# Performance work log

Hardware: AMD Instinct MI355X
Metric: run time of the kernel (lower is better)

Reference implementation:

```python
import jax, jax.numpy as jnp
import numpy as np

DIM = 192
HEADS = 6
HD = DIM // HEADS
MEM = 8
EMA = 0.99
MLP_H = int(DIM * 2.0)
SCALE = HD ** -0.5
EPS = 1e-5


def layer_norm(x, w, b):
    mu = x.mean(-1, keepdims=True)
    xc = x - mu
    var = (xc * xc).mean(-1, keepdims=True)
    return xc * jax.lax.rsqrt(var + EPS) * w + b


def setup_inputs() -> dict:
    key = jax.random.key(0)
    ks = jax.random.split(key, 16)
    B, H, W = 2, 96, 96
    x = jax.random.normal(ks[0], (B, H * W, DIM), jnp.float32)

    def lin(k, din, dout):
        kw, kb = jax.random.split(k)
        return (0.02 * jax.random.normal(kw, (din, dout), jnp.float32),
                0.02 * jax.random.normal(kb, (dout,), jnp.float32))

    wq, bq = lin(ks[1], DIM, DIM)
    wk, bk = lin(ks[2], DIM, DIM)
    wv, bv = lin(ks[3], DIM, DIM)
    wo, bo = lin(ks[4], DIM, DIM)
    w1, b1 = lin(ks[5], DIM, MLP_H)
    w2, b2 = lin(ks[6], MLP_H, DIM)
    ones = jnp.ones((DIM,), jnp.float32)
    zeros = jnp.zeros((DIM,), jnp.float32)
    return dict(x_bnc=x,
                ln_q_w=ones, ln_q_b=zeros,
                ln_kv_w=ones, ln_kv_b=zeros,
                wq=wq, bq=bq, wk=wk, bk=bk, wv=wv, bv=bv,
                wo=wo, bo=bo,
                ln2_w=ones, ln2_b=zeros,
                w1=w1, b1=b1, w2=w2, b2=b2,
                H=96, W=96)


def reference(x_bnc, ln_q_w, ln_q_b, ln_kv_w, ln_kv_b,
              wq, bq, wk, bk, wv, bv, wo, bo,
              ln2_w, ln2_b, w1, b1, w2, b2, H, W):
    B, N, C = x_bnc.shape

    # --- memory init (fresh module: _mem_init is False) ---
    # mem_k = mean token over batch+tokens, replicated to MEM slots; mem_v = 0
    mem_k = jax.lax.stop_gradient(jnp.mean(x_bnc, axis=(0, 1)))          # (C,)
    mem_k = jnp.broadcast_to(mem_k, (1, MEM, C))
    mem_v = jnp.zeros((1, MEM, C), x_bnc.dtype)

    # --- 2x2 average-pool downsample (count_include_pad irrelevant: no pad) ---
    x_dn = (x_bnc.reshape(B, H, W, C)
                 .reshape(B, H // 2, 2, W // 2, 2, C)
                 .mean(axis=(2, 4))
                 .reshape(B, (H // 2) * (W // 2), C))                    # (B, T, C)
    T = x_dn.shape[1]

    # --- projections ---
    q = layer_norm(x_bnc, ln_q_w, ln_q_b) @ wq + bq                      # (B, N, C)
    kv = layer_norm(x_dn, ln_kv_w, ln_kv_b)
    k_new = kv @ wk + bk                                                 # (B, T, C)
    v_new = kv @ wv + bv

    # --- EMA memory update (no-grad, adaptive avg pool T->MEM = bin means) ---
    k_bar = jax.lax.stop_gradient(k_new.reshape(B, MEM, T // MEM, C).mean(axis=2).mean(axis=0))
    v_bar = jax.lax.stop_gradient(v_new.reshape(B, MEM, T // MEM, C).mean(axis=2).mean(axis=0))
    mem_k = EMA * mem_k + (1.0 - EMA) * k_bar[None]                      # (1, MEM, C)
    mem_v = EMA * mem_v + (1.0 - EMA) * v_bar[None]

    # --- concat memory slots onto KV ---
    k_cat = jnp.concatenate([k_new, jnp.broadcast_to(mem_k, (B, MEM, C))], axis=1)
    v_cat = jnp.concatenate([v_new, jnp.broadcast_to(mem_v, (B, MEM, C))], axis=1)

    # --- multi-head attention (explicit scores) ---
    qh = q.reshape(B, N, HEADS, HD)
    kh = k_cat.reshape(B, T + MEM, HEADS, HD)
    vh = v_cat.reshape(B, T + MEM, HEADS, HD)
    attn = jnp.einsum('bqhd,bkhd->bhqk', qh * SCALE, kh)                 # (B, H, N, T+M)
    attn = jax.nn.softmax(attn, axis=-1)
    out = jnp.einsum('bhqk,bkhd->bqhd', attn, vh).reshape(B, N, C)
    out = out @ wo + bo

    # --- post MLP with residual (exact erf GELU, as torch default) ---
    h = layer_norm(out, ln2_w, ln2_b)
    out = out + (jax.nn.gelu(h @ w1 + b1, approximate=False) @ w2 + b2)
    return out
```

## Files before the change

kernel.cpp:

```cpp
#include <hip/hip_runtime.h>
#include <hip/hip_bf16.h>
#include <math.h>

#define B_    2
#define N_    9216
#define C_    192
#define HD_   32
#define T_    2304
#define MEM_  8
#define TK_   2312
#define TKP_  2336
#define NPAD_ 24
#define MLPH_ 384
#define SCALE_ 0.17677669529663687f
#define QSCALE_ 0.25504167229218905f
#define EPS_  1e-5f

typedef __bf16 v8bf __attribute__((ext_vector_type(8)));
typedef __bf16 v4bf __attribute__((ext_vector_type(4)));
typedef float  v4f  __attribute__((ext_vector_type(4)));

#define MFMA16(a, b, c) __builtin_amdgcn_mfma_f32_16x16x32_bf16((a), (b), (c), 0, 0, 0)

static __device__ __forceinline__ float gelu_erf(float x) {
    return 0.5f * x * (1.0f + erff(x * 0.70710678118654752f));
}

__global__ void k_rowpart(const float* __restrict__ x, float* __restrict__ part) {
    int j = threadIdx.x;
    const float* p = x + (size_t)blockIdx.x * 128 * C_;
    float s = 0.f;
    for (int r = 0; r < 128; ++r) s += p[r * C_ + j];
    part[blockIdx.x * C_ + j] = s;
}

__global__ void k_meanfin(const float* __restrict__ part, float* __restrict__ meanx) {
    int j = threadIdx.x;
    float s = 0.f;
    for (int i = 0; i < 144; ++i) s += part[i * C_ + j];
    meanx[j] = s * (1.0f / 18432.0f);
}

__global__ __launch_bounds__(256) void k_prep(const float* __restrict__ wq,
                       const float* __restrict__ wk,
                       const float* __restrict__ wv, const float* __restrict__ wo,
                       const float* __restrict__ w1, const float* __restrict__ w2,
                       __bf16* __restrict__ wqT, __bf16* __restrict__ wkT,
                       __bf16* __restrict__ wvT, __bf16* __restrict__ woT,
                       __bf16* __restrict__ w1T, __bf16* __restrict__ w2T) {
    __shared__ float tile[32][33];
    int b = blockIdx.x;
    const float* src; __bf16* dst; int K, Nn, t0;
    if (b < 144)      { int m = b / 36; t0 = b % 36;
                        src = m==0?wq:m==1?wk:m==2?wv:wo;
                        dst = m==0?wqT:m==1?wkT:m==2?wvT:woT; K=192; Nn=192; }
    else if (b < 216) { t0 = b - 144; src = w1; dst = w1T; K=192; Nn=384; }
    else              { t0 = b - 216; src = w2; dst = w2T; K=384; Nn=192; }
    int ntn = Nn / 32;
    int k0 = (t0 / ntn) * 32, n0 = (t0 % ntn) * 32;
    int r = threadIdx.x >> 5, c = threadIdx.x & 31;
#pragma unroll
    for (int i = 0; i < 4; ++i)
        tile[r + i * 8][c] = src[(size_t)(k0 + r + i * 8) * Nn + n0 + c];
    __syncthreads();
#pragma unroll
    for (int i = 0; i < 4; ++i)
        dst[(size_t)(n0 + r + i * 8) * K + k0 + c] = (__bf16)tile[c][r + i * 8];
}

__global__ __launch_bounds__(256) void k_qproj(const float* __restrict__ x,
        const float* __restrict__ lnw, const float* __restrict__ lnb,
        const __bf16* __restrict__ wqT, const float* __restrict__ bq,
        __bf16* __restrict__ q) {
    __shared__ float  Of[32][196];
    __shared__ __bf16 Abf[32][200];
    __shared__ float  mu_s[32], rs_s[32];
    int tid = threadIdx.x;
    int w = tid >> 6, lane = tid & 63, qi = lane & 15, g = lane >> 4;
    size_t row0 = (size_t)blockIdx.x * 32;

    for (int e = tid; e < 32 * 48; e += 256) {
        int r = e / 48, c4 = e % 48;
        *(float4*)&Of[r][c4 * 4] = *(const float4*)(x + (row0 + r) * C_ + c4 * 4);
    }
    __syncthreads();
    {
        int r = tid >> 3, part = tid & 7;
        float s = 0.f, ss = 0.f;
        for (int i = 0; i < 24; ++i) { float a = Of[r][part * 24 + i]; s += a; ss += a * a; }
        s += __shfl_xor(s, 1); ss += __shfl_xor(ss, 1);
        s += __shfl_xor(s, 2); ss += __shfl_xor(ss, 2);
        s += __shfl_xor(s, 4); ss += __shfl_xor(ss, 4);
        if (part == 0) {
            float m = s * (1.f / C_);
            float var = ss * (1.f / C_) - m * m;
            mu_s[r] = m; rs_s[r] = rsqrtf(var + EPS_);
        }
    }
    __syncthreads();
    {
        int r = tid >> 3, part = tid & 7;
        float m = mu_s[r], rv = rs_s[r];
        for (int i = 0; i < 24; ++i) {
            int c = part * 24 + i;
            Abf[r][c] = (__bf16)((Of[r][c] - m) * rv * lnw[c] + lnb[c]);
        }
    }
    __syncthreads();

    v4f acc[2][3];
#pragma unroll
    for (int m = 0; m < 2; ++m)
#pragma unroll
        for (int n = 0; n < 3; ++n) acc[m][n] = (v4f){0.f, 0.f, 0.f, 0.f};
#pragma unroll
    for (int kk = 0; kk < 6; ++kk) {
        v8bf a0 = *(const v8bf*)&Abf[qi][kk * 32 + g * 8];
        v8bf a1 = *(const v8bf*)&Abf[16 + qi][kk * 32 + g * 8];
#pragma unroll
        for (int n = 0; n < 3; ++n) {
            v8bf bfr = *(const v8bf*)(wqT + (size_t)(w * 48 + n * 16 + qi) * C_ + kk * 32 + g * 8);
            acc[0][n] = MFMA16(a0, bfr, acc[0][n]);
            acc[1][n] = MFMA16(a1, bfr, acc[1][n]);
        }
    }
#pragma unroll
    for (int n = 0; n < 3; ++n) {
        int col = w * 48 + n * 16 + qi;
        float bb = bq[col];
#pragma unroll
        for (int m = 0; m < 2; ++m)
#pragma unroll
            for (int r = 0; r < 4; ++r)
                q[(row0 + m * 16 + g * 4 + r) * C_ + col] = (__bf16)((acc[m][n][r] + bb) * QSCALE_);
    }
}

__global__ __launch_bounds__(256) void k_kvproj(const float* __restrict__ x,
        const float* __restrict__ lnw, const float* __restrict__ lnb,
        const __bf16* __restrict__ wkT, const float* __restrict__ bk,
        const __bf16* __restrict__ wvT, const float* __restrict__ bv,
        __bf16* __restrict__ kcat, __bf16* __restrict__ vTr) {
    __shared__ float  Of[32][196];
    __shared__ __bf16 Abf[32][200];
    __shared__ float  mu_s[32], rs_s[32];
    int tid = threadIdx.x;
    int w = tid >> 6, lane = tid & 63, qi = lane & 15, g = lane >> 4;
    int p0 = blockIdx.x * 32;
    int bbb = p0 / T_, tbase = p0 % T_;

    for (int e = tid; e < 32 * 48; e += 256) {
        int r = e / 48, c4 = e % 48;
        int t = tbase + r;
        int h2 = t / 48, w2c = t % 48;
        const float* s0 = x + ((size_t)bbb * N_ + (size_t)(2 * h2) * 96 + 2 * w2c) * C_ + c4 * 4;
        float4 u0 = *(const float4*)(s0);
        float4 u1 = *(const float4*)(s0 + C_);
        float4 u2 = *(const float4*)(s0 + 96 * C_);
        float4 u3 = *(const float4*)(s0 + 96 * C_ + C_);
        float4 a;
        a.x = 0.25f * (u0.x + u1.x + u2.x + u3.x);
        a.y = 0.25f * (u0.y + u1.y + u2.y + u3.y);
        a.z = 0.25f * (u0.z + u1.z + u2.z + u3.z);
        a.w = 0.25f * (u0.w + u1.w + u2.w + u3.w);
        *(float4*)&Of[r][c4 * 4] = a;
    }
    __syncthreads();
    {
        int r = tid >> 3, part = tid & 7;
        float s = 0.f, ss = 0.f;
        for (int i = 0; i < 24; ++i) { float a = Of[r][part * 24 + i]; s += a; ss += a * a; }
        s += __shfl_xor(s, 1); ss += __shfl_xor(ss, 1);
        s += __shfl_xor(s, 2); ss += __shfl_xor(ss, 2);
        s += __shfl_xor(s, 4); ss += __shfl_xor(ss, 4);
        if (part == 0) {
            float m = s * (1.f / C_);
            float var = ss * (1.f / C_) - m * m;
            mu_s[r] = m; rs_s[r] = rsqrtf(var + EPS_);
        }
    }
    __syncthreads();
    {
        int r = tid >> 3, part = tid & 7;
        float m = mu_s[r], rv = rs_s[r];
        for (int i = 0; i < 24; ++i) {
            int c = part * 24 + i;
            Abf[r][c] = (__bf16)((Of[r][c] - m) * rv * lnw[c] + lnb[c]);
        }
    }
    __syncthreads();

    v4f ak[2][3], av[2][3];
#pragma unroll
    for (int m = 0; m < 2; ++m)
#pragma unroll
        for (int n = 0; n < 3; ++n) { ak[m][n] = (v4f){0.f,0.f,0.f,0.f}; av[m][n] = (v4f){0.f,0.f,0.f,0.f}; }
#pragma unroll
    for (int kk = 0; kk < 6; ++kk) {
        v8bf a0 = *(const v8bf*)&Abf[qi][kk * 32 + g * 8];
        v8bf a1 = *(const v8bf*)&Abf[16 + qi][kk * 32 + g * 8];
#pragma unroll
        for (int n = 0; n < 3; ++n) {
            int col = w * 48 + n * 16 + qi;
            v8bf bk8 = *(const v8bf*)(wkT + (size_t)col * C_ + kk * 32 + g * 8);
            v8bf bv8 = *(const v8bf*)(wvT + (size_t)col * C_ + kk * 32 + g * 8);
            ak[0][n] = MFMA16(a0, bk8, ak[0][n]);
            ak[1][n] = MFMA16(a1, bk8, ak[1][n]);
            av[0][n] = MFMA16(a0, bv8, av[0][n]);
            av[1][n] = MFMA16(a1, bv8, av[1][n]);
        }
    }
#pragma unroll
    for (int n = 0; n < 3; ++n) {
        int col = w * 48 + n * 16 + qi;
        float bkc = bk[col], bvc = bv[col];
        int hh = col >> 5, dd = col & 31;
        size_t vrow = ((size_t)(bbb * 6 + hh) * HD_ + dd) * TKP_;
#pragma unroll
        for (int m = 0; m < 2; ++m) {
            v4bf vv;
#pragma unroll
            for (int r = 0; r < 4; ++r) {
                int t = tbase + m * 16 + g * 4 + r;
                size_t row = (size_t)bbb * TKP_ + t;
                kcat[row * C_ + col] = (__bf16)(ak[m][n][r] + bkc);
                vv[r] = (__bf16)(av[m][n][r] + bvc);
            }
            *(v4bf*)(vTr + vrow + tbase + g * 8 + m * 4) = vv;
        }
    }
}

__global__ void k_mempart(const __bf16* __restrict__ kcat, const __bf16* __restrict__ vTr,
                          float* __restrict__ kp, float* __restrict__ vp) {
    int m = blockIdx.x, ch = blockIdx.y, j = threadIdx.x;
    int hh = j >> 5, dd = j & 31;
    float sk = 0.f, sv = 0.f;
    for (int bb = 0; bb < 2; ++bb) {
        const __bf16* kpp = kcat + ((size_t)bb * TKP_ + m * 288 + ch * 24) * C_ + j;
        for (int t = 0; t < 24; ++t) sk += (float)kpp[t * C_];
        const __bf16* p = vTr + ((size_t)(bb * 6 + hh) * HD_ + dd) * TKP_ + m * 288 + ch * 24;
        for (int t = 0; t < 24; t += 8) {
            v8bf v = *(const v8bf*)(p + t);
#pragma unroll
            for (int u = 0; u < 8; ++u) sv += (float)v[u];
        }
    }
    kp[(m * 12 + ch) * C_ + j] = sk;
    vp[(m * 12 + ch) * C_ + j] = sv;
}

__global__ void k_memfin(const float* __restrict__ meanx,
                         const float* __restrict__ kp, const float* __restrict__ vp,
                         __bf16* __restrict__ kcat, __bf16* __restrict__ vTr) {
    int m = blockIdx.x, j = threadIdx.x;
    int hh = j >> 5, dd = j & 31;
    if (m < 8) {
        float sk = 0.f, sv = 0.f;
        for (int ch = 0; ch < 12; ++ch) {
            sk += kp[(m * 12 + ch) * C_ + j];
            sv += vp[(m * 12 + ch) * C_ + j];
        }
        float mk = 0.99f * meanx[j] + 0.01f * sk * (1.0f / 576.0f);
        float mv = sv * (0.01f / 576.0f);
        for (int bb = 0; bb < 2; ++bb)
            kcat[((size_t)bb * TKP_ + T_ + m) * C_ + j] = (__bf16)mk;
        int slot = (m >> 2) * 8 + (m & 3);
        for (int bb = 0; bb < 2; ++bb)
            vTr[((size_t)(bb * 6 + hh) * HD_ + dd) * TKP_ + T_ + slot] = (__bf16)mv;
    } else {
        int t32 = m;
        int slot = (t32 < 16) ? ((t32 >> 2) * 8 + (t32 & 3))
                              : (((t32 >> 2) - 4) * 8 + 4 + (t32 & 3));
        for (int bb = 0; bb < 2; ++bb) {
            kcat[((size_t)bb * TKP_ + TK_ + (m - 8)) * C_ + j] = (__bf16)0.f;
            vTr[((size_t)(bb * 6 + hh) * HD_ + dd) * TKP_ + T_ + slot] = (__bf16)0.f;
        }
    }
}

__global__ __launch_bounds__(256) void k_attn(const __bf16* __restrict__ q,
                                              const __bf16* __restrict__ kc,
                                              const __bf16* __restrict__ vt,
                                              __bf16* __restrict__ po,
                                              float* __restrict__ psb) {
    int tid = threadIdx.x;
    int w = tid >> 6, lane = tid & 63, g = lane >> 4, qi = lane & 15;
    int bs = blockIdx.z;
    int bb = bs >> 2, sp = bs & 3;
    int h = blockIdx.y;
    int qt = blockIdx.x * 256 + w * 64;
    int kv_lo = sp * 576;
    int kv_hi = (sp == 3) ? TKP_ : kv_lo + 576;
    const size_t BNC = (size_t)B_ * N_ * C_;

    v8bf qf[4];
#pragma unroll
    for (int t = 0; t < 4; ++t)
        qf[t] = *(const v8bf*)(q + ((size_t)bb * N_ + qt + t * 16 + qi) * C_ + h * HD_ + g * 8);

    v4f o0[4], o1[4], ps[4];
#pragma unroll
    for (int t = 0; t < 4; ++t) {
        o0[t] = (v4f){0.f,0.f,0.f,0.f};
        o1[t] = (v4f){0.f,0.f,0.f,0.f};
        ps[t] = (v4f){0.f,0.f,0.f,0.f};
    }
    v8bf ones;
#pragma unroll
    for (int i = 0; i < 8; ++i) ones[i] = (__bf16)1.0f;

    const __bf16* kbase = kc + ((size_t)bb * TKP_ + qi) * C_ + h * HD_ + g * 8;
    const __bf16* vb0 = vt + ((size_t)((bb * 6 + h) * HD_) + qi) * TKP_ + g * 8;
    const __bf16* vb1 = vb0 + (size_t)16 * TKP_;

    for (int kv0 = kv_lo; kv0 < kv_hi; kv0 += 32) {
        v8bf kf0 = *(const v8bf*)(kbase + (size_t)kv0 * C_);
        v8bf kf1 = *(const v8bf*)(kbase + (size_t)(kv0 + 16) * C_);
        v8bf va0 = *(const v8bf*)(vb0 + kv0);
        v8bf va1 = *(const v8bf*)(vb1 + kv0);
        v4f z = {0.f,0.f,0.f,0.f};
#pragma unroll
        for (int t = 0; t < 4; ++t) {
            v4f s0 = MFMA16(kf0, qf[t], z);
            v4f s1 = MFMA16(kf1, qf[t], z);
            v8bf pb;
#pragma unroll
            for (int r = 0; r < 4; ++r) {
                pb[r]     = (__bf16)__builtin_amdgcn_exp2f(s0[r]);
                pb[4 + r] = (__bf16)__builtin_amdgcn_exp2f(s1[r]);
            }
            o0[t] = MFMA16(va0, pb, o0[t]);
            o1[t] = MFMA16(va1, pb, o1[t]);
            ps[t] = MFMA16(ones, pb, ps[t]);
        }
    }

    __bf16* pbase = po + (size_t)sp * BNC;
#pragma unroll
    for (int t = 0; t < 4; ++t) {
        __bf16* orow = pbase + ((size_t)bb * N_ + qt + t * 16 + qi) * C_ + h * HD_;
        v4bf a, b;
#pragma unroll
        for (int r = 0; r < 4; ++r) { a[r] = (__bf16)o0[t][r]; b[r] = (__bf16)o1[t][r]; }
        *(v4bf*)(orow + g * 4)      = a;
        *(v4bf*)(orow + 16 + g * 4) = b;
    }
    if (lane < 16) {
#pragma unroll
        for (int t = 0; t < 4; ++t)
            psb[((size_t)bs * 6 + h) * N_ + qt + t * 16 + qi] = ps[t][0];
    }
}

__global__ __launch_bounds__(256) void k_post(const __bf16* __restrict__ po,
        const float* __restrict__ psb,
        const __bf16* __restrict__ woT, const float* __restrict__ bo,
        const float* __restrict__ ln2w, const float* __restrict__ ln2b,
        const __bf16* __restrict__ w1T, const float* __restrict__ b1,
        const __bf16* __restrict__ w2T, const float* __restrict__ b2,
        float* __restrict__ out) {
    __shared__ __bf16 Abf[32][200];
    __shared__ __bf16 H[32][392];
    __shared__ float  partLN[4][32][2];
    __shared__ float  mu_s[32], rs_s[32];
    __shared__ float  inv_s[32][6];
    int tid = threadIdx.x;
    int w = tid >> 6, lane = tid & 63, qi = lane & 15, g = lane >> 4;
    size_t row0 = (size_t)blockIdx.x * 32;
    const size_t BNC = (size_t)B_ * N_ * C_;

    if (tid < 192) {
        int r = tid / 6, h = tid % 6;
        size_t n = row0 + r;
        int bb = (n >= N_) ? 1 : 0;
        int nn = (int)(n - (size_t)bb * N_);
        float s = -(float)NPAD_;
#pragma unroll
        for (int sp = 0; sp < 4; ++sp)
            s += psb[((size_t)(bb * 4 + sp) * 6 + h) * N_ + nn];
        inv_s[r][h] = 1.f / s;
    }
    __syncthreads();

    for (int e = tid; e < 32 * 48; e += 256) {
        int r = e / 48, c4 = e % 48;
        float iv = inv_s[r][c4 >> 3];
        size_t n = row0 + r;
        float acc[4] = {0.f, 0.f, 0.f, 0.f};
#pragma unroll
        for (int sp = 0; sp < 4; ++sp) {
            v4bf v = *(const v4bf*)(po + (size_t)sp * BNC + n * C_ + c4 * 4);
#pragma unroll
            for (int u = 0; u < 4; ++u) acc[u] += (float)v[u];
        }
        v4bf pbf;
#pragma unroll
        for (int u = 0; u < 4; ++u) pbf[u] = (__bf16)(acc[u] * iv);
        *(v4bf*)&Abf[r][c4 * 4] = pbf;
    }
    __syncthreads();

    v4f acc1[2][3];
#pragma unroll
    for (int m = 0; m < 2; ++m)
#pragma unroll
        for (int n = 0; n < 3; ++n) acc1[m][n] = (v4f){0.f,0.f,0.f,0.f};
#pragma unroll
    for (int kk = 0; kk < 6; ++kk) {
        v8bf a0 = *(const v8bf*)&Abf[qi][kk * 32 + g * 8];
        v8bf a1 = *(const v8bf*)&Abf[16 + qi][kk * 32 + g * 8];
#pragma unroll
        for (int n = 0; n < 3; ++n) {
            v8bf bfr = *(const v8bf*)(woT + (size_t)(w * 48 + n * 16 + qi) * C_ + kk * 32 + g * 8);
            acc1[0][n] = MFMA16(a0, bfr, acc1[0][n]);
            acc1[1][n] = MFMA16(a1, bfr, acc1[1][n]);
        }
    }
#pragma unroll
    for (int n = 0; n < 3; ++n) {
        float bb = bo[w * 48 + n * 16 + qi];
#pragma unroll
        for (int m = 0; m < 2; ++m)
#pragma unroll
            for (int r = 0; r < 4; ++r) acc1[m][n][r] += bb;
    }

    {
        float sr[2][4], qr[2][4];
#pragma unroll
        for (int m = 0; m < 2; ++m)
#pragma unroll
            for (int r = 0; r < 4; ++r) {
                float s = acc1[m][0][r] + acc1[m][1][r] + acc1[m][2][r];
                float q2 = acc1[m][0][r] * acc1[m][0][r] + acc1[m][1][r] * acc1[m][1][r]
                         + acc1[m][2][r] * acc1[m][2][r];
                s += __shfl_xor(s, 1); q2 += __shfl_xor(q2, 1);
                s += __shfl_xor(s, 2); q2 += __shfl_xor(q2, 2);
                s += __shfl_xor(s, 4); q2 += __shfl_xor(q2, 4);
                s += __shfl_xor(s, 8); q2 += __shfl_xor(q2, 8);
                sr[m][r] = s; qr[m][r] = q2;
            }
        if (qi == 0) {
#pragma unroll
            for (int m = 0; m < 2; ++m)
#pragma unroll
                for (int r = 0; r < 4; ++r) {
                    partLN[w][m * 16 + g * 4 + r][0] = sr[m][r];
                    partLN[w][m * 16 + g * 4 + r][1] = qr[m][r];
                }
        }
    }
    __syncthreads();
    if (tid < 32) {
        float s  = partLN[0][tid][0] + partLN[1][tid][0] + partLN[2][tid][0] + partLN[3][tid][0];
        float q2 = partLN[0][tid][1] + partLN[1][tid][1] + partLN[2][tid][1] + partLN[3][tid][1];
        float mm = s * (1.f / C_);
        float var = q2 * (1.f / C_) - mm * mm;
        mu_s[tid] = mm; rs_s[tid] = rsqrtf(var + EPS_);
    }
    __syncthreads();
#pragma unroll
    for (int n = 0; n < 3; ++n) {
        int col = w * 48 + n * 16 + qi;
        float lw = ln2w[col], lb = ln2b[col];
#pragma unroll
        for (int m = 0; m < 2; ++m)
#pragma unroll
            for (int r = 0; r < 4; ++r) {
                int row = m * 16 + g * 4 + r;
                Abf[row][col] = (__bf16)((acc1[m][n][r] - mu_s[row]) * rs_s[row] * lw + lb);
            }
    }
    __syncthreads();

    v4f acc2[2][6];
#pragma unroll
    for (int m = 0; m < 2; ++m)
#pragma unroll
        for (int n = 0; n < 6; ++n) acc2[m][n] = (v4f){0.f,0.f,0.f,0.f};
#pragma unroll
    for (int kk = 0; kk < 6; ++kk) {
        v8bf a0 = *(const v8bf*)&Abf[qi][kk * 32 + g * 8];
        v8bf a1 = *(const v8bf*)&Abf[16 + qi][kk * 32 + g * 8];
#pragma unroll
        for (int n = 0; n < 6; ++n) {
            v8bf bfr = *(const v8bf*)(w1T + (size_t)(w * 96 + n * 16 + qi) * C_ + kk * 32 + g * 8);
            acc2[0][n] = MFMA16(a0, bfr, acc2[0][n]);
            acc2[1][n] = MFMA16(a1, bfr, acc2[1][n]);
        }
    }
#pragma unroll
    for (int n = 0; n < 6; ++n) {
        int col = w * 96 + n * 16 + qi;
        float bb = b1[col];
#pragma unroll
        for (int m = 0; m < 2; ++m)
#pragma unroll
            for (int r = 0; r < 4; ++r)
                H[m * 16 + g * 4 + r][col] = (__bf16)gelu_erf(acc2[m][n][r] + bb);
    }
    __syncthreads();

    v4f acc3[2][3];
#pragma unroll
    for (int m = 0; m < 2; ++m)
#pragma unroll
        for (int n = 0; n < 3; ++n) acc3[m][n] = (v4f){0.f,0.f,0.f,0.f};
#pragma unroll
    for (int kk = 0; kk < 12; ++kk) {
        v8bf a0 = *(const v8bf*)&H[qi][kk * 32 + g * 8];
        v8bf a1 = *(const v8bf*)&H[16 + qi][kk * 32 + g * 8];
#pragma unroll
        for (int n = 0; n < 3; ++n) {
            v8bf bfr = *(const v8bf*)(w2T + (size_t)(w * 48 + n * 16 + qi) * MLPH_ + kk * 32 + g * 8);
            acc3[0][n] = MFMA16(a0, bfr, acc3[0][n]);
            acc3[1][n] = MFMA16(a1, bfr, acc3[1][n]);
        }
    }
#pragma unroll
    for (int n = 0; n < 3; ++n) {
        int col = w * 48 + n * 16 + qi;
        float bb = b2[col];
#pragma unroll
        for (int m = 0; m < 2; ++m)
#pragma unroll
            for (int r = 0; r < 4; ++r)
                out[(row0 + m * 16 + g * 4 + r) * C_ + col] = acc1[m][n][r] + acc3[m][n][r] + bb;
    }
}

extern "C" void kernel_launch(void* const* d_in, const int* in_sizes, int n_in,
                              void* d_out, int out_size, void* d_ws, size_t ws_size,
                              hipStream_t stream) {
    const float* x    = (const float*)d_in[0];
    const float* lnqw = (const float*)d_in[1];
    const float* lnqb = (const float*)d_in[2];
    const float* lnkw = (const float*)d_in[3];
    const float* lnkb = (const float*)d_in[4];
    const float* wq   = (const float*)d_in[5];
    const float* bq   = (const float*)d_in[6];
    const float* wk   = (const float*)d_in[7];
    const float* bk   = (const float*)d_in[8];
    const float* wv   = (const float*)d_in[9];
    const float* bv   = (const float*)d_in[10];
    const float* wo   = (const float*)d_in[11];
    const float* bo   = (const float*)d_in[12];
    const float* ln2w = (const float*)d_in[13];
    const float* ln2b = (const float*)d_in[14];
    const float* w1   = (const float*)d_in[15];
    const float* b1   = (const float*)d_in[16];
    const float* w2   = (const float*)d_in[17];
    const float* b2   = (const float*)d_in[18];

    char* w0 = (char*)d_ws;
    const size_t QB  = (size_t)B_ * N_ * C_ * 2;
    const size_t KVB = (size_t)B_ * TKP_ * C_ * 2;
    const size_t POB = (size_t)4 * B_ * N_ * C_ * 2;
    __bf16* qb  = (__bf16*)(w0);
    __bf16* kcb = (__bf16*)(w0 + QB);
    __bf16* vtr = (__bf16*)(w0 + QB + KVB);
    __bf16* po  = (__bf16*)(w0 + QB + 2 * KVB);
    float*  psb = (float*) (w0 + QB + 2 * KVB + POB);
    float*  kp    = psb + (size_t)8 * 6 * N_;
    float*  vp    = kp + 96 * C_;
    float*  part  = vp + 96 * C_;
    float*  meanx = part + 144 * C_;
    char* wbase = (char*)(meanx + 192 + 32);
    wbase = (char*)(((uintptr_t)wbase + 255) & ~(uintptr_t)255);
    __bf16* wqT = (__bf16*)(wbase);
    __bf16* wkT = wqT + 36864;
    __bf16* wvT = wkT + 36864;
    __bf16* woT = wvT + 36864;
    __bf16* w1T = woT + 36864;
    __bf16* w2T = w1T + 73728;

    hipLaunchKernelGGL(k_prep, dim3(288), dim3(256), 0, stream,
                       wq, wk, wv, wo, w1, w2, wqT, wkT, wvT, woT, w1T, w2T);
    hipLaunchKernelGGL(k_rowpart, dim3(144), dim3(192), 0, stream, x, part);
    hipLaunchKernelGGL(k_meanfin, dim3(1), dim3(192), 0, stream, part, meanx);
    hipLaunchKernelGGL(k_kvproj, dim3(144), dim3(256), 0, stream,
                       x, lnkw, lnkb, wkT, bk, wvT, bv, kcb, vtr);
    hipLaunchKernelGGL(k_mempart, dim3(8, 12), dim3(192), 0, stream, kcb, vtr, kp, vp);
    hipLaunchKernelGGL(k_memfin, dim3(32), dim3(192), 0, stream, meanx, kp, vp, kcb, vtr);
    hipLaunchKernelGGL(k_qproj, dim3(576), dim3(256), 0, stream,
                       x, lnqw, lnqb, wqT, bq, qb);
    hipLaunchKernelGGL(k_attn, dim3(36, 6, 8), dim3(256), 0, stream,
                       qb, kcb, vtr, po, psb);
    hipLaunchKernelGGL(k_post, dim3(576), dim3(256), 0, stream,
                       po, psb, woT, bo, ln2w, ln2b, w1T, b1, w2T, b2, (float*)d_out);
}
```

Measured before the change: 151.4 us.

## Merge prologue kernels into three launches and shrink attention blocks to one wave

Folds the weight transpose and row partial sums into one kernel, the mean finalize into the KV projection kernel as an extra block, and the memory partial sums into the Q projection kernel. This cuts the number of small launches and their serialization gaps in the prologue. The attention kernel now runs one 64-thread wave per block over 64 query rows, with four times as many blocks, which should improve scheduling granularity and tail balance. The risk is that single-wave blocks can no longer share anything between waves, and the fused kernels carry some idle extra threads.

Result: faster. 139.8 us (-7.7%).

```diff
diff --git a/kernel.cpp b/kernel.cpp
--- a/kernel.cpp
+++ b/kernel.cpp
@@ -26,121 +26,59 @@
     return 0.5f * x * (1.0f + erff(x * 0.70710678118654752f));
 }
 
-__global__ void k_rowpart(const float* __restrict__ x, float* __restrict__ part) {
-    int j = threadIdx.x;
-    const float* p = x + (size_t)blockIdx.x * 128 * C_;
-    float s = 0.f;
-    for (int r = 0; r < 128; ++r) s += p[r * C_ + j];
-    part[blockIdx.x * C_ + j] = s;
-}
-
-__global__ void k_meanfin(const float* __restrict__ part, float* __restrict__ meanx) {
-    int j = threadIdx.x;
-    float s = 0.f;
-    for (int i = 0; i < 144; ++i) s += part[i * C_ + j];
-    meanx[j] = s * (1.0f / 18432.0f);
-}
-
-__global__ __launch_bounds__(256) void k_prep(const float* __restrict__ wq,
+__global__ __launch_bounds__(256) void k_pre1(const float* __restrict__ wq,
                        const float* __restrict__ wk,
                        const float* __restrict__ wv, const float* __restrict__ wo,
                        const float* __restrict__ w1, const float* __restrict__ w2,
                        __bf16* __restrict__ wqT, __bf16* __restrict__ wkT,
                        __bf16* __restrict__ wvT, __bf16* __restrict__ woT,
-                       __bf16* __restrict__ w1T, __bf16* __restrict__ w2T) {
+                       __bf16* __restrict__ w1T, __bf16* __restrict__ w2T,
+                       const float* __restrict__ x, float* __restrict__ part) {
     __shared__ float tile[32][33];
     int b = blockIdx.x;
-    const float* src; __bf16* dst; int K, Nn, t0;
-    if (b < 144)      { int m = b / 36; t0 = b % 36;
-                        src = m==0?wq:m==1?wk:m==2?wv:wo;
-                        dst = m==0?wqT:m==1?wkT:m==2?wvT:woT; K=192; Nn=192; }
-    else if (b < 216) { t0 = b - 144; src = w1; dst = w1T; K=192; Nn=384; }
-    else              { t0 = b - 216; src = w2; dst = w2T; K=384; Nn=192; }
-    int ntn = Nn / 32;
-    int k0 = (t0 / ntn) * 32, n0 = (t0 % ntn) * 32;
-    int r = threadIdx.x >> 5, c = threadIdx.x & 31;
-#pragma unroll
-    for (int i = 0; i < 4; ++i)
-        tile[r + i * 8][c] = src[(size_t)(k0 + r + i * 8) * Nn + n0 + c];
-    __syncthreads();
-#pragma unroll
-    for (int i = 0; i < 4; ++i)
-        dst[(size_t)(n0 + r + i * 8) * K + k0 + c] = (__bf16)tile[c][r + i * 8];
-}
-
-__global__ __launch_bounds__(256) void k_qproj(const float* __restrict__ x,
-        const float* __restrict__ lnw, const float* __restrict__ lnb,
-        const __bf16* __restrict__ wqT, const float* __restrict__ bq,
-        __bf16* __restrict__ q) {
-    __shared__ float  Of[32][196];
-    __shared__ __bf16 Abf[32][200];
-    __shared__ float  mu_s[32], rs_s[32];
-    int tid = threadIdx.x;
-    int w = tid >> 6, lane = tid & 63, qi = lane & 15, g = lane >> 4;
-    size_t row0 = (size_t)blockIdx.x * 32;
-
-    for (int e = tid; e < 32 * 48; e += 256) {
-        int r = e / 48, c4 = e % 48;
-        *(float4*)&Of[r][c4 * 4] = *(const float4*)(x + (row0 + r) * C_ + c4 * 4);
-    }
-    __syncthreads();
-    {
-        int r = tid >> 3, part = tid & 7;
-        float s = 0.f, ss = 0.f;
-        for (int i = 0; i < 24; ++i) { float a = Of[r][part * 24 + i]; s += a; ss += a * a; }
-        s += __shfl_xor(s, 1); ss += __shfl_xor(ss, 1);
-        s += __shfl_xor(s, 2); ss += __shfl_xor(ss, 2);
-        s += __shfl_xor(s, 4); ss += __shfl_xor(ss, 4);
-        if (part == 0) {
-            float m = s * (1.f / C_);
-            float var = ss * (1.f / C_) - m * m;
-            mu_s[r] = m; rs_s[r] = rsqrtf(var + EPS_);
-        }
-    }
-    __syncthreads();
-    {
-        int r = tid >> 3, part = tid & 7;
-        float m = mu_s[r], rv = rs_s[r];
-        for (int i = 0; i < 24; ++i) {
-            int c = part * 24 + i;
-            Abf[r][c] = (__bf16)((Of[r][c] - m) * rv * lnw[c] + lnb[c]);
-        }
-    }
-    __syncthreads();
-
-    v4f acc[2][3];
-#pragma unroll
-    for (int m = 0; m < 2; ++m)
-#pragma unroll
-        for (int n = 0; n < 3; ++n) acc[m][n] = (v4f){0.f, 0.f, 0.f, 0.f};
-#pragma unroll
-    for (int kk = 0; kk < 6; ++kk) {
-        v8bf a0 = *(const v8bf*)&Abf[qi][kk * 32 + g * 8];
-        v8bf a1 = *(const v8bf*)&Abf[16 + qi][kk * 32 + g * 8];
-#pragma unroll
-        for (int n = 0; n < 3; ++n) {
-            v8bf bfr = *(const v8bf*)(wqT + (size_t)(w * 48 + n * 16 + qi) * C_ + kk * 32 + g * 8);
-            acc[0][n] = MFMA16(a0, bfr, acc[0][n]);
-            acc[1][n] = MFMA16(a1, bfr, acc[1][n]);
-        }
-    }
-#pragma unroll
-    for (int n = 0; n < 3; ++n) {
-        int col = w * 48 + n * 16 + qi;
-        float bb = bq[col];
-#pragma unroll
-        for (int m = 0; m < 2; ++m)
-#pragma unroll
-            for (int r = 0; r < 4; ++r)
-                q[(row0 + m * 16 + g * 4 + r) * C_ + col] = (__bf16)((acc[m][n][r] + bb) * QSCALE_);
-    }
-}
-
-__global__ __launch_bounds__(256) void k_kvproj(const float* __restrict__ x,
+    if (b < 288) {
+        const float* src; __bf16* dst; int K, Nn, t0;
+        if (b < 144)      { int m = b / 36; t0 = b % 36;
+                            src = m==0?wq:m==1?wk:m==2?wv:wo;
+                            dst = m==0?wqT:m==1?wkT:m==2?wvT:woT; K=192; Nn=192; }
+        else if (b < 216) { t0 = b - 144; src = w1; dst = w1T; K=192; Nn=384; }
+        else              { t0 = b - 216; src = w2; dst = w2T; K=384; Nn=192; }
+        int ntn = Nn / 32;
+        int k0 = (t0 / ntn) * 32, n0 = (t0 % ntn) * 32;
+        int r = threadIdx.x >> 5, c = threadIdx.x & 31;
+#pragma unroll
+        for (int i = 0; i < 4; ++i)
+            tile[r + i * 8][c] = src[(size_t)(k0 + r + i * 8) * Nn + n0 + c];
+        __syncthreads();
+#pragma unroll
+        for (int i = 0; i < 4; ++i)
+            dst[(size_t)(n0 + r + i * 8) * K + k0 + c] = (__bf16)tile[c][r + i * 8];
+    } else {
+        int j = threadIdx.x;
+        if (j < 192) {
+            const float* p = x + (size_t)(b - 288) * 128 * C_;
+            float s = 0.f;
+            for (int r = 0; r < 128; ++r) s += p[r * C_ + j];
+            part[(b - 288) * C_ + j] = s;
+        }
+    }
+}
+
+__global__ __launch_bounds__(256) void k_pre2(const float* __restrict__ x,
         const float* __restrict__ lnw, const float* __restrict__ lnb,
         const __bf16* __restrict__ wkT, const float* __restrict__ bk,
         const __bf16* __restrict__ wvT, const float* __restrict__ bv,
-        __bf16* __restrict__ kcat, __bf16* __restrict__ vTr) {
+        __bf16* __restrict__ kcat, __bf16* __restrict__ vTr,
+        const float* __restrict__ part, float* __restrict__ meanx) {
+    if (blockIdx.x == 144) {
+        int j = threadIdx.x;
+        if (j < 192) {
+            float s = 0.f;
+            for (int i = 0; i < 144; ++i) s += part[i * C_ + j];
+            meanx[j] = s * (1.0f / 18432.0f);
+        }
+        return;
+    }
     __shared__ float  Of[32][196];
     __shared__ __bf16 Abf[32][200];
     __shared__ float  mu_s[32], rs_s[32];
@@ -167,13 +105,13 @@
     }
     __syncthreads();
     {
-        int r = tid >> 3, part = tid & 7;
+        int r = tid >> 3, part8 = tid & 7;
         float s = 0.f, ss = 0.f;
-        for (int i = 0; i < 24; ++i) { float a = Of[r][part * 24 + i]; s += a; ss += a * a; }
+        for (int i = 0; i < 24; ++i) { float a = Of[r][part8 * 24 + i]; s += a; ss += a * a; }
         s += __shfl_xor(s, 1); ss += __shfl_xor(ss, 1);
         s += __shfl_xor(s, 2); ss += __shfl_xor(ss, 2);
         s += __shfl_xor(s, 4); ss += __shfl_xor(ss, 4);
-        if (part == 0) {
+        if (part8 == 0) {
             float m = s * (1.f / C_);
             float var = ss * (1.f / C_) - m * m;
             mu_s[r] = m; rs_s[r] = rsqrtf(var + EPS_);
@@ -181,10 +119,10 @@
     }
     __syncthreads();
     {
-        int r = tid >> 3, part = tid & 7;
+        int r = tid >> 3, part8 = tid & 7;
         float m = mu_s[r], rv = rs_s[r];
         for (int i = 0; i < 24; ++i) {
-            int c = part * 24 + i;
+            int c = part8 * 24 + i;
             Abf[r][c] = (__bf16)((Of[r][c] - m) * rv * lnw[c] + lnb[c]);
         }
     }
@@ -231,23 +169,96 @@
     }
 }
 
-__global__ void k_mempart(const __bf16* __restrict__ kcat, const __bf16* __restrict__ vTr,
-                          float* __restrict__ kp, float* __restrict__ vp) {
-    int m = blockIdx.x, ch = blockIdx.y, j = threadIdx.x;
-    int hh = j >> 5, dd = j & 31;
-    float sk = 0.f, sv = 0.f;
-    for (int bb = 0; bb < 2; ++bb) {
-        const __bf16* kpp = kcat + ((size_t)bb * TKP_ + m * 288 + ch * 24) * C_ + j;
-        for (int t = 0; t < 24; ++t) sk += (float)kpp[t * C_];
-        const __bf16* p = vTr + ((size_t)(bb * 6 + hh) * HD_ + dd) * TKP_ + m * 288 + ch * 24;
-        for (int t = 0; t < 24; t += 8) {
-            v8bf v = *(const v8bf*)(p + t);
-#pragma unroll
-            for (int u = 0; u < 8; ++u) sv += (float)v[u];
-        }
-    }
-    kp[(m * 12 + ch) * C_ + j] = sk;
-    vp[(m * 12 + ch) * C_ + j] = sv;
+__global__ __launch_bounds__(256) void k_pre3(const float* __restrict__ x,
+        const float* __restrict__ lnw, const float* __restrict__ lnb,
+        const __bf16* __restrict__ wqT, const float* __restrict__ bq,
+        __bf16* __restrict__ q,
+        const __bf16* __restrict__ kcat, const __bf16* __restrict__ vTr,
+        float* __restrict__ kp, float* __restrict__ vp) {
+    if (blockIdx.x >= 576) {
+        int e = blockIdx.x - 576;
+        int m = e / 12, ch = e % 12;
+        int j = threadIdx.x;
+        if (j < 192) {
+            int hh = j >> 5, dd = j & 31;
+            float sk = 0.f, sv = 0.f;
+            for (int bb = 0; bb < 2; ++bb) {
+                const __bf16* kpp = kcat + ((size_t)bb * TKP_ + m * 288 + ch * 24) * C_ + j;
+                for (int t = 0; t < 24; ++t) sk += (float)kpp[t * C_];
+                const __bf16* p = vTr + ((size_t)(bb * 6 + hh) * HD_ + dd) * TKP_ + m * 288 + ch * 24;
+                for (int t = 0; t < 24; t += 8) {
+                    v8bf v = *(const v8bf*)(p + t);
+#pragma unroll
+                    for (int u = 0; u < 8; ++u) sv += (float)v[u];
+                }
+            }
+            kp[(m * 12 + ch) * C_ + j] = sk;
+            vp[(m * 12 + ch) * C_ + j] = sv;
+        }
+        return;
+    }
+    __shared__ float  Of[32][196];
+    __shared__ __bf16 Abf[32][200];
+    __shared__ float  mu_s[32], rs_s[32];
+    int tid = threadIdx.x;
+    int w = tid >> 6, lane = tid & 63, qi = lane & 15, g = lane >> 4;
+    size_t row0 = (size_t)blockIdx.x * 32;
+
+    for (int e = tid; e < 32 * 48; e += 256) {
+        int r = e / 48, c4 = e % 48;
+        *(float4*)&Of[r][c4 * 4] = *(const float4*)(x + (row0 + r) * C_ + c4 * 4);
+    }
+    __syncthreads();
+    {
+        int r = tid >> 3, part8 = tid & 7;
+        float s = 0.f, ss = 0.f;
+        for (int i = 0; i < 24; ++i) { float a = Of[r][part8 * 24 + i]; s += a; ss += a * a; }
+        s += __shfl_xor(s, 1); ss += __shfl_xor(ss, 1);
+        s += __shfl_xor(s, 2); ss += __shfl_xor(ss, 2);
+        s += __shfl_xor(s, 4); ss += __shfl_xor(ss, 4);
+        if (part8 == 0) {
+            float m = s * (1.f / C_);
+            float var = ss * (1.f / C_) - m * m;
+            mu_s[r] = m; rs_s[r] = rsqrtf(var + EPS_);
+        }
+    }
+    __syncthreads();
+    {
+        int r = tid >> 3, part8 = tid & 7;
+        float m = mu_s[r], rv = rs_s[r];
+        for (int i = 0; i < 24; ++i) {
+            int c = part8 * 24 + i;
+            Abf[r][c] = (__bf16)((Of[r][c] - m) * rv * lnw[c] + lnb[c]);
+        }
+    }
+    __syncthreads();
+
+    v4f acc[2][3];
+#pragma unroll
+    for (int m = 0; m < 2; ++m)
+#pragma unroll
+        for (int n = 0; n < 3; ++n) acc[m][n] = (v4f){0.f, 0.f, 0.f, 0.f};
+#pragma unroll
+    for (int kk = 0; kk < 6; ++kk) {
+        v8bf a0 = *(const v8bf*)&Abf[qi][kk * 32 + g * 8];
+        v8bf a1 = *(const v8bf*)&Abf[16 + qi][kk * 32 + g * 8];
+#pragma unroll
+        for (int n = 0; n < 3; ++n) {
+            v8bf bfr = *(const v8bf*)(wqT + (size_t)(w * 48 + n * 16 + qi) * C_ + kk * 32 + g * 8);
+            acc[0][n] = MFMA16(a0, bfr, acc[0][n]);
+            acc[1][n] = MFMA16(a1, bfr, acc[1][n]);
+        }
+    }
+#pragma unroll
+    for (int n = 0; n < 3; ++n) {
+        int col = w * 48 + n * 16 + qi;
+        float bb = bq[col];
+#pragma unroll
+        for (int m = 0; m < 2; ++m)
+#pragma unroll
+            for (int r = 0; r < 4; ++r)
+                q[(row0 + m * 16 + g * 4 + r) * C_ + col] = (__bf16)((acc[m][n][r] + bb) * QSCALE_);
+    }
 }
 
 __global__ void k_memfin(const float* __restrict__ meanx,
@@ -279,17 +290,16 @@
     }
 }
 
-__global__ __launch_bounds__(256) void k_attn(const __bf16* __restrict__ q,
-                                              const __bf16* __restrict__ kc,
-                                              const __bf16* __restrict__ vt,
-                                              __bf16* __restrict__ po,
-                                              float* __restrict__ psb) {
-    int tid = threadIdx.x;
-    int w = tid >> 6, lane = tid & 63, g = lane >> 4, qi = lane & 15;
+__global__ __launch_bounds__(64) void k_attn(const __bf16* __restrict__ q,
+                                             const __bf16* __restrict__ kc,
+                                             const __bf16* __restrict__ vt,
+                                             __bf16* __restrict__ po,
+                                             float* __restrict__ psb) {
+    int lane = threadIdx.x & 63, g = lane >> 4, qi = lane & 15;
     int bs = blockIdx.z;
     int bb = bs >> 2, sp = bs & 3;
     int h = blockIdx.y;
-    int qt = blockIdx.x * 256 + w * 64;
+    int qt = blockIdx.x * 64;
     int kv_lo = sp * 576;
     int kv_hi = (sp == 3) ? TKP_ : kv_lo + 576;
     const size_t BNC = (size_t)B_ * N_ * C_;
@@ -575,17 +585,14 @@
     __bf16* w1T = woT + 36864;
     __bf16* w2T = w1T + 73728;
 
-    hipLaunchKernelGGL(k_prep, dim3(288), dim3(256), 0, stream,
-                       wq, wk, wv, wo, w1, w2, wqT, wkT, wvT, woT, w1T, w2T);
-    hipLaunchKernelGGL(k_rowpart, dim3(144), dim3(192), 0, stream, x, part);
-    hipLaunchKernelGGL(k_meanfin, dim3(1), dim3(192), 0, stream, part, meanx);
-    hipLaunchKernelGGL(k_kvproj, dim3(144), dim3(256), 0, stream,
-                       x, lnkw, lnkb, wkT, bk, wvT, bv, kcb, vtr);
-    hipLaunchKernelGGL(k_mempart, dim3(8, 12), dim3(192), 0, stream, kcb, vtr, kp, vp);
+    hipLaunchKernelGGL(k_pre1, dim3(432), dim3(256), 0, stream,
+                       wq, wk, wv, wo, w1, w2, wqT, wkT, wvT, woT, w1T, w2T, x, part);
+    hipLaunchKernelGGL(k_pre2, dim3(145), dim3(256), 0, stream,
+                       x, lnkw, lnkb, wkT, bk, wvT, bv, kcb, vtr, part, meanx);
+    hipLaunchKernelGGL(k_pre3, dim3(672), dim3(256), 0, stream,
+                       x, lnqw, lnqb, wqT, bq, qb, kcb, vtr, kp, vp);
     hipLaunchKernelGGL(k_memfin, dim3(32), dim3(192), 0, stream, meanx, kp, vp, kcb, vtr);
-    hipLaunchKernelGGL(k_qproj, dim3(576), dim3(256), 0, stream,
-                       x, lnqw, lnqb, wqT, bq, qb);
-    hipLaunchKernelGGL(k_attn, dim3(36, 6, 8), dim3(256), 0, stream,
+    hipLaunchKernelGGL(k_attn, dim3(144, 6, 8), dim3(64), 0, stream,
                        qb, kcb, vtr, po, psb);
     hipLaunchKernelGGL(k_post, dim3(576), dim3(256), 0, stream,
                        po, psb, woT, bo, ln2w, ln2b, w1T, b1, w2T, b2, (float*)d_out);
```
